# Performance work log

Hardware: AMD Instinct MI355X
Metric: run time of the kernel (lower is better)

The kernel has to match this reference:

```python
import jax, jax.numpy as jnp
import numpy as np

B = 4096
OBS, ACT, RDIM = 128, 32, 4
HID = 1024                      # embedding output / head hidden dim
DIMS = [OBS + ACT + RDIM, 128, 128, RDIM]   # target net: 164 -> 128 -> 128 -> 4
N_LAYERS = len(DIMS) - 1


def setup_inputs() -> dict:
    key = jax.random.key(0)
    ks = iter(jax.random.split(key, 64))

    def p(shape, scale=0.02):
        return jax.random.normal(next(ks), shape, jnp.float32) * scale

    inp = {
        "obs": jax.random.normal(next(ks), (B, OBS), jnp.float32),
        "action": jax.random.normal(next(ks), (B, ACT), jnp.float32),
        "prefs": jax.random.uniform(next(ks), (B, RDIM), jnp.float32),
        # embedding MLP (hypernet): (obs, prefs) -> z
        "We1": p((OBS + RDIM, HID)), "be1": jnp.zeros((HID,), jnp.float32),
        "We2": p((HID, HID)), "be2": jnp.zeros((HID,), jnp.float32),
    }
    # head nets: per target layer, linear heads emitting weight / bias / scale
    for i in range(N_LAYERS):
        din, dout = DIMS[i], DIMS[i + 1]
        inp[f"Ww{i}"] = p((HID, dout * din))
        inp[f"bw{i}"] = jnp.zeros((dout * din,), jnp.float32)
        inp[f"Wb{i}"] = p((HID, dout))
        inp[f"bb{i}"] = jnp.zeros((dout,), jnp.float32)
        inp[f"Ws{i}"] = p((HID, dout))
        inp[f"bs{i}"] = jnp.ones((dout,), jnp.float32)  # scale ~ 1 at init
    return inp


def reference(obs, action, prefs, We1, be1, We2, be2,
              Ww0, bw0, Wb0, bb0, Ws0, bs0,
              Ww1, bw1, Wb1, bb1, Ws1, bs1,
              Ww2, bw2, Wb2, bb2, Ws2, bs2):
    # hypernet embedding z  (hypernet_inputs = [obs, prefs])
    hin = jnp.concatenate([obs, prefs], axis=-1)          # [B, 132]
    z = jax.nn.relu(hin @ We1 + be1)
    z = jax.nn.relu(z @ We2 + be2)                        # [B, HID]

    heads = [(Ww0, bw0, Wb0, bb0, Ws0, bs0),
             (Ww1, bw1, Wb1, bb1, Ws1, bs1),
             (Ww2, bw2, Wb2, bb2, Ws2, bs2)]

    # target network input (target_net_inputs = [obs, action, prefs])
    x = jnp.concatenate([obs, action, prefs], axis=-1)    # [B, 164]

    for i, (Ww, bw, Wb, bb, Ws, bs) in enumerate(heads):
        din, dout = DIMS[i], DIMS[i + 1]
        w = (z @ Ww + bw).reshape(-1, dout, din)          # per-sample [B, dout, din]
        b = z @ Wb + bb                                   # [B, dout]
        s = z @ Ws + bs                                   # [B, dout]
        x = (jnp.einsum('bi,boi->bo', x, w) + b) * s      # batched matmul+bias+scale
        if i < N_LAYERS - 1:                              # activation_mask: all but last
            x = jax.nn.relu(x)
    return x                                              # [B, reward_dim]
```

## Files before the change

### kernel.cpp

```cpp
#include <hip/hip_runtime.h>
#include <hip/hip_bf16.h>
#include <stdint.h>

#define B4 4096
#define KZ 1088
#define KH 160

typedef short bf16x8 __attribute__((ext_vector_type(8)));
typedef float f32x4 __attribute__((ext_vector_type(4)));

__device__ __forceinline__ float b2f(uint16_t u){
  union {float f; uint32_t i;} v; v.i = ((uint32_t)u)<<16; return v.f;
}
__device__ __forceinline__ uint16_t f2b(float f){
  union {float fv; uint32_t i;} v; v.fv = f;
  uint32_t r = v.i + 0x7FFFu + ((v.i>>16)&1u);
  return (uint16_t)(r>>16);
}
__device__ __forceinline__ void gload16(const void* g, void* l){
  __builtin_amdgcn_global_load_lds(
      (__attribute__((address_space(1))) void*)(g),
      (__attribute__((address_space(3))) void*)(l), 16, 0, 0);
}

__global__ __launch_bounds__(256) void transpose_pack(
    const float* __restrict__ src, const float* __restrict__ bias,
    uint16_t* __restrict__ dst,
    int Ncols, int Kdst, int Ksrc, int src_ld, int din_dst, int din_src)
{
  __shared__ float tile[32][33];
  int ct = blockIdx.x, kt = blockIdx.y;
  int tid = threadIdx.x;
  int cl = tid & 31, kg = tid >> 5;
  #pragma unroll
  for (int r = 0; r < 4; ++r){
    int kl = kg*4 + r;
    int k  = kt*32 + kl;
    int c  = ct*32 + cl;
    float v = 0.f;
    if (c < Ncols){
      int o = c / din_dst, i = c - o*din_dst;
      if (i < din_src){
        int sc = o*din_src + i;
        if (k < Ksrc)       v = src[(size_t)k*src_ld + sc];
        else if (k == Ksrc) v = bias[sc];
      }
    }
    tile[kl][cl] = v;
  }
  __syncthreads();
  int c_loc = tid >> 3, kq = tid & 7;
  int c = ct*32 + c_loc;
  if (c < Ncols){
    ushort4 st;
    uint16_t* sp = (uint16_t*)&st;
    #pragma unroll
    for (int r = 0; r < 4; ++r) sp[r] = f2b(tile[kq*4 + r][c_loc]);
    *(ushort4*)&dst[(size_t)c*Kdst + kt*32 + kq*4] = st;
  }
}

__global__ __launch_bounds__(256) void pack_hin(
    const float* __restrict__ obs, const float* __restrict__ prefs,
    uint16_t* __restrict__ hinp)
{
  int idx = blockIdx.x*256 + threadIdx.x;
  int b = idx / KH, k = idx - b*KH;
  float v;
  if (k < 128)      v = obs[b*128 + k];
  else if (k < 132) v = prefs[b*4 + (k-128)];
  else              v = (k == 132) ? 1.f : 0.f;
  hinp[idx] = f2b(v);
}

__global__ __launch_bounds__(256) void pack_x0T(
    const float* __restrict__ obs, const float* __restrict__ act,
    const float* __restrict__ prefs, uint16_t* __restrict__ x0T)
{
  int idx = blockIdx.x*256 + threadIdx.x;
  int c = idx >> 12;
  int b = idx & (B4-1);
  float v = 0.f;
  if (c < 128)      v = obs[b*128 + c];
  else if (c < 160) v = act[b*32 + (c-128)];
  else if (c < 164) v = prefs[b*4 + (c-160)];
  x0T[idx] = f2b(v);
}

__global__ __launch_bounds__(256) void zinit(uint16_t* __restrict__ z1p,
                                             uint16_t* __restrict__ zp)
{
  int idx = blockIdx.x*256 + threadIdx.x;
  int t = idx & 127;
  int row = idx >> 7;
  uint16_t* p = (t < 64) ? z1p : zp;
  int col = 1024 + (t & 63);
  p[(size_t)row*KZ + col] = ((t & 63) == 0) ? (uint16_t)0x3F80 : (uint16_t)0;
}

template<int RELU, int OUTBF, int TRANS>
__global__ __launch_bounds__(256) void gemm128(
    const uint16_t* __restrict__ A, int lda,
    const uint16_t* __restrict__ BT, int ldb,
    void* __restrict__ Cv, int ldc, int K)
{
  __shared__ char smA[128*64];
  __shared__ char smB[128*64];
  int tid = threadIdx.x, w = tid >> 6, lane = tid & 63;
  int m0 = blockIdx.x*128, n0 = blockIdx.y*128;
  const uint16_t* Ab = A  + (size_t)m0*lda;
  const uint16_t* Bb = BT + (size_t)n0*ldb;
  f32x4 acc[2][8];
  #pragma unroll
  for (int mf = 0; mf < 2; ++mf)
    #pragma unroll
    for (int nf = 0; nf < 8; ++nf) acc[mf][nf] = (f32x4){0.f,0.f,0.f,0.f};
  int colg = lane & 15, hi = lane >> 4;

  for (int k0 = 0; k0 < K; k0 += 32){
    #pragma unroll
    for (int p = 0; p < 2; ++p){
      int rb = p*4 + w;
      int row = rb*16 + (lane >> 2);
      int chunk = (lane & 3) ^ ((row >> 1) & 3);
      gload16(Ab + (size_t)row*lda + k0 + chunk*8, &smA[rb*1024]);
      gload16(Bb + (size_t)row*ldb + k0 + chunk*8, &smB[rb*1024]);
    }
    __syncthreads();
    bf16x8 af[2];
    #pragma unroll
    for (int mf = 0; mf < 2; ++mf){
      int row = w*32 + mf*16 + colg;
      af[mf] = *(const bf16x8*)&smA[row*64 + ((hi ^ ((row>>1)&3)) << 4)];
    }
    #pragma unroll
    for (int nf = 0; nf < 8; ++nf){
      int row = nf*16 + colg;
      bf16x8 bfr = *(const bf16x8*)&smB[row*64 + ((hi ^ ((row>>1)&3)) << 4)];
      acc[0][nf] = __builtin_amdgcn_mfma_f32_16x16x32_bf16(af[0], bfr, acc[0][nf], 0,0,0);
      acc[1][nf] = __builtin_amdgcn_mfma_f32_16x16x32_bf16(af[1], bfr, acc[1][nf], 0,0,0);
    }
    __syncthreads();
  }
  #pragma unroll
  for (int mf = 0; mf < 2; ++mf){
    #pragma unroll
    for (int nf = 0; nf < 8; ++nf){
      int col = n0 + nf*16 + colg;
      #pragma unroll
      for (int r = 0; r < 4; ++r){
        int row = m0 + w*32 + mf*16 + hi*4 + r;
        float v = acc[mf][nf][r];
        if (RELU) v = v > 0.f ? v : 0.f;
        if (TRANS)      ((float*)Cv)[(size_t)col*ldc + row] = v;
        else if (OUTBF) ((uint16_t*)Cv)[(size_t)row*ldc + col] = f2b(v);
        else            ((float*)Cv)[(size_t)row*ldc + col] = v;
      }
    }
  }
}

template<int DINP>
__global__ __launch_bounds__(512, 2) void hyper2n(
    const uint16_t* __restrict__ zp,
    const uint16_t* __restrict__ WpT,
    const uint16_t* __restrict__ xT,
    const float*  __restrict__ bsbT,
    uint16_t* __restrict__ outT,
    int relu)
{
  constexpr int NF     = DINP/32;
  constexpr int BCALLS = DINP/64;
  constexpr int WAITN  = 2 + BCALLS;
  constexpr int HBUF   = 16384 + 2*DINP*64;
  constexpr int NH     = KZ/32;
  __shared__ char sm[3*HBUF];

  int tid = threadIdx.x, w = tid >> 6, lane = tid & 63;
  int wm = w >> 2, wn = w & 3;
  int f = blockIdx.x;
  int xcd = f & 7;
  int j = f >> 3;
  int pair = j >> 1;
  int mt = xcd*2 + (j & 1);
  int m0 = mt*256;
  const uint16_t* Ag = zp  + (size_t)m0*KZ;
  const uint16_t* Bg = WpT + (size_t)pair*(2*DINP)*KZ;
  int colg = lane & 15, hi = lane >> 4;

  f32x4 acc[8][NF];
  #pragma unroll
  for (int mf = 0; mf < 8; ++mf)
    #pragma unroll
    for (int nf = 0; nf < NF; ++nf) acc[mf][nf] = (f32x4){0.f,0.f,0.f,0.f};

  auto SA = [&](int h, int a){
    int row = a*128 + (tid >> 2);
    int ch  = (tid & 3) ^ ((row >> 1) & 3);
    gload16(Ag + (size_t)row*KZ + h*32 + ch*8,
            sm + (h%3)*HBUF + a*8192 + w*1024);
  };
  auto SB = [&](int h, int b){
    int row = b*128 + (tid >> 2);
    int ch  = (tid & 3) ^ ((row >> 1) & 3);
    gload16(Bg + (size_t)row*KZ + h*32 + ch*8,
            sm + (h%3)*HBUF + 16384 + b*8192 + w*1024);
  };

  SA(0,0); SA(0,1);
  #pragma unroll
  for (int b = 0; b < BCALLS; ++b) SB(0,b);
  SA(1,0); SA(1,1);
  #pragma unroll
  for (int b = 0; b < BCALLS; ++b) SB(1,b);

  for (int h = 0; h < NH; ++h){
    const char* base = sm + (h%3)*HBUF;
    if (h == NH-1) asm volatile("s_waitcnt vmcnt(0)" ::: "memory");
    else           asm volatile("s_waitcnt vmcnt(%0)" :: "i"(WAITN) : "memory");
    __builtin_amdgcn_s_barrier();
    if (h + 2 < NH){
      SA(h+2,0); SA(h+2,1);
      #pragma unroll
      for (int b = 0; b < BCALLS; ++b) SB(h+2,b);
    }
    bf16x8 Bf[NF];
    #pragma unroll
    for (int nf = 0; nf < NF; ++nf){
      int rc = wn*(DINP/2) + nf*16 + colg;
      Bf[nf] = *(const bf16x8*)(base + 16384 + rc*64 + ((hi ^ ((rc>>1)&3)) << 4));
    }
    #pragma unroll
    for (int m = 0; m < 8; ++m){
      int row = wm*128 + m*16 + colg;
      bf16x8 a = *(const bf16x8*)(base + row*64 + ((hi ^ ((row>>1)&3)) << 4));
      #pragma unroll
      for (int nf = 0; nf < NF; ++nf)
        acc[m][nf] = __builtin_amdgcn_mfma_f32_16x16x32_bf16(a, Bf[nf], acc[m][nf], 0,0,0);
    }
  }

  __syncthreads();
  float* red = (float*)sm;
  int parity = wn & 1, o_loc = wn >> 1;
  #pragma unroll
  for (int mf = 0; mf < 8; ++mf){
    float p0=0.f, p1=0.f, p2=0.f, p3=0.f;
    int b0 = m0 + wm*128 + mf*16 + hi*4;
    #pragma unroll
    for (int nf = 0; nf < NF; ++nf){
      int il = parity*(DINP/2) + nf*16 + colg;
      ushort4 xv = *(const ushort4*)(xT + (size_t)il*B4 + b0);
      f32x4 a = acc[mf][nf];
      p0 += a[0]*b2f(xv.x); p1 += a[1]*b2f(xv.y);
      p2 += a[2]*b2f(xv.z); p3 += a[3]*b2f(xv.w);
    }
    #pragma unroll
    for (int off = 1; off < 16; off <<= 1){
      p0 += __shfl_xor(p0, off); p1 += __shfl_xor(p1, off);
      p2 += __shfl_xor(p2, off); p3 += __shfl_xor(p3, off);
    }
    if (colg == 0){
      int rloc = wm*128 + mf*16 + hi*4;
      float* rp = red + parity*512 + o_loc*256 + rloc;
      rp[0] = p0; rp[1] = p1; rp[2] = p2; rp[3] = p3;
    }
  }
  __syncthreads();
  {
    int o_l = tid >> 8, row = tid & 255;
    int o = pair*2 + o_l;
    float v = red[o_l*256 + row] + red[512 + o_l*256 + row];
    float bv = bsbT[(size_t)o*B4 + m0 + row];
    float sv = bsbT[(size_t)(128+o)*B4 + m0 + row];
    float val = (v + bv) * sv;
    if (relu) val = val > 0.f ? val : 0.f;
    outT[(size_t)o*B4 + m0 + row] = f2b(val);
  }
}

__global__ __launch_bounds__(256) void finalize_k(
    const float* __restrict__ w2, const uint16_t* __restrict__ x2T,
    const float* __restrict__ bs2, float* __restrict__ out)
{
  int tid = threadIdx.x;
  int o = tid & 3;
  int b = blockIdx.x*64 + (tid >> 2);
  const float* wr = w2 + (size_t)b*512 + o*128;
  float dot = 0.f;
  #pragma unroll
  for (int i = 0; i < 128; i += 4){
    float4 wv = *(const float4*)(wr + i);
    dot += wv.x * b2f(x2T[(size_t)(i+0)*B4 + b]);
    dot += wv.y * b2f(x2T[(size_t)(i+1)*B4 + b]);
    dot += wv.z * b2f(x2T[(size_t)(i+2)*B4 + b]);
    dot += wv.w * b2f(x2T[(size_t)(i+3)*B4 + b]);
  }
  float bv = bs2[(size_t)b*128 + o];
  float sv = bs2[(size_t)b*128 + 4 + o];
  out[b*4 + o] = (dot + bv) * sv;
}

extern "C" void kernel_launch(void* const* d_in, const int* in_sizes, int n_in,
                              void* d_out, int out_size, void* d_ws, size_t ws_size,
                              hipStream_t stream)
{
  const float* obs   = (const float*)d_in[0];
  const float* act   = (const float*)d_in[1];
  const float* prefs = (const float*)d_in[2];
  const float* We1 = (const float*)d_in[3];
  const float* be1 = (const float*)d_in[4];
  const float* We2 = (const float*)d_in[5];
  const float* be2 = (const float*)d_in[6];
  const float* Ww0 = (const float*)d_in[7],  *bw0 = (const float*)d_in[8];
  const float* Wb0 = (const float*)d_in[9],  *bb0 = (const float*)d_in[10];
  const float* Ws0 = (const float*)d_in[11], *bs0i = (const float*)d_in[12];
  const float* Ww1 = (const float*)d_in[13], *bw1 = (const float*)d_in[14];
  const float* Wb1 = (const float*)d_in[15], *bb1 = (const float*)d_in[16];
  const float* Ws1 = (const float*)d_in[17], *bs1i = (const float*)d_in[18];
  const float* Ww2 = (const float*)d_in[19], *bw2 = (const float*)d_in[20];
  const float* Wb2 = (const float*)d_in[21], *bb2 = (const float*)d_in[22];
  const float* Ws2 = (const float*)d_in[23], *bs2i = (const float*)d_in[24];

  char* ws = (char*)d_ws;
  size_t off = 0;
  auto alloc = [&](size_t bytes)->char*{
    char* p = ws + off; off += (bytes + 255) & ~(size_t)255; return p;
  };
  uint16_t* WpT0  = (uint16_t*)alloc((size_t)24576*KZ*2);
  uint16_t* WpT1  = (uint16_t*)alloc((size_t)16384*KZ*2);
  uint16_t* WpT2  = (uint16_t*)alloc((size_t)512*KZ*2);
  uint16_t* We1T  = (uint16_t*)alloc((size_t)1024*KH*2);
  uint16_t* We2T  = (uint16_t*)alloc((size_t)1024*KZ*2);
  uint16_t* Wbs0T = (uint16_t*)alloc((size_t)256*KZ*2);
  uint16_t* Wbs1T = (uint16_t*)alloc((size_t)256*KZ*2);
  uint16_t* Wbs2T = (uint16_t*)alloc((size_t)128*KZ*2);
  uint16_t* hinp  = (uint16_t*)alloc((size_t)B4*KH*2);
  uint16_t* z1p   = (uint16_t*)alloc((size_t)B4*KZ*2);
  uint16_t* zp    = (uint16_t*)alloc((size_t)B4*KZ*2);
  float*    bsb0  = (float*)alloc((size_t)256*B4*4);
  float*    bsb1  = (float*)alloc((size_t)256*B4*4);
  float*    bsb2  = (float*)alloc((size_t)B4*128*4);
  uint16_t* x0T   = (uint16_t*)alloc((size_t)192*B4*2);
  uint16_t* x1T   = (uint16_t*)alloc((size_t)128*B4*2);
  uint16_t* x2T   = (uint16_t*)alloc((size_t)128*B4*2);
  float*    w2    = (float*)alloc((size_t)B4*512*4);
  (void)ws_size; (void)in_sizes; (void)n_in; (void)out_size;

  hipMemsetAsync(Wbs2T, 0, (size_t)128*KZ*2, stream);

  dim3 blk(256);
  auto tg = [](int nc, int kd){ return dim3((nc+31)/32, kd/32); };
  transpose_pack<<<tg(24576,KZ),blk,0,stream>>>(Ww0, bw0, WpT0, 24576, KZ, 1024, 20992, 192, 164);
  transpose_pack<<<tg(16384,KZ),blk,0,stream>>>(Ww1, bw1, WpT1, 16384, KZ, 1024, 16384, 128, 128);
  transpose_pack<<<tg(512,KZ),blk,0,stream>>>(Ww2, bw2, WpT2, 512, KZ, 1024, 512, 128, 128);
  transpose_pack<<<tg(1024,KH),blk,0,stream>>>(We1, be1, We1T, 1024, KH, 132, 1024, 1024, 1024);
  transpose_pack<<<tg(1024,KZ),blk,0,stream>>>(We2, be2, We2T, 1024, KZ, 1024, 1024, 1024, 1024);
  transpose_pack<<<tg(128,KZ),blk,0,stream>>>(Wb0, bb0, Wbs0T,          128, KZ, 1024, 128, 128, 128);
  transpose_pack<<<tg(128,KZ),blk,0,stream>>>(Ws0, bs0i, Wbs0T + 128*KZ,128, KZ, 1024, 128, 128, 128);
  transpose_pack<<<tg(128,KZ),blk,0,stream>>>(Wb1, bb1, Wbs1T,          128, KZ, 1024, 128, 128, 128);
  transpose_pack<<<tg(128,KZ),blk,0,stream>>>(Ws1, bs1i, Wbs1T + 128*KZ,128, KZ, 1024, 128, 128, 128);
  transpose_pack<<<tg(4,KZ),blk,0,stream>>>(Wb2, bb2, Wbs2T,        4, KZ, 1024, 4, 4, 4);
  transpose_pack<<<tg(4,KZ),blk,0,stream>>>(Ws2, bs2i, Wbs2T + 4*KZ,4, KZ, 1024, 4, 4, 4);

  pack_hin<<<dim3(B4*KH/256),blk,0,stream>>>(obs, prefs, hinp);
  pack_x0T<<<dim3(192*B4/256),blk,0,stream>>>(obs, act, prefs, x0T);
  zinit<<<dim3(B4*128/256),blk,0,stream>>>(z1p, zp);

  gemm128<1,1,0><<<dim3(32,8),blk,0,stream>>>(hinp, KH, We1T, KH, z1p, KZ, KH);
  gemm128<1,1,0><<<dim3(32,8),blk,0,stream>>>(z1p, KZ, We2T, KZ, zp, KZ, KZ);
  gemm128<0,0,1><<<dim3(32,4),blk,0,stream>>>(zp, KZ, Wbs0T, KZ, bsb0, B4, KZ);
  gemm128<0,0,0><<<dim3(32,1),blk,0,stream>>>(zp, KZ, Wbs2T, KZ, bsb2, 128, KZ);

  hyper2n<192><<<dim3(1024),dim3(512),0,stream>>>(zp, WpT0, x0T, bsb0, x1T, 1);
  hyper2n<128><<<dim3(1024),dim3(512),0,stream>>>(zp, WpT1, x1T, bsb1, x2T, 1);

  gemm128<0,0,0><<<dim3(32,4),blk,0,stream>>>(zp, KZ, WpT2, KZ, w2, 512, KZ);
  finalize_k<<<dim3(B4/64),blk,0,stream>>>(w2, x2T, bsb2, (float*)d_out);
}
```

Baseline: 603.2 us.

## Shrink padded K, merge packing kernels, and precompute hyper2n load addresses

Reduces the padded inner dimension KZ from 1088 to 1056, cutting the wasted K work and bytes in every z-based GEMM. It also merges the six small bias/scale transpose launches into one kernel, and the three input-packing launches into one. The hyper2n main loop now uses precomputed pointers and LDS offsets with a 3-way unrolled ring buffer, replacing the per-iteration address math. Risks: NH must be divisible by 3 for the unrolled loop, Wbs1T is no longer written, and correctness depends on the bias layout still matching hyper2n.

```diff
diff --git a/kernel.cpp b/kernel.cpp
--- a/kernel.cpp
+++ b/kernel.cpp
@@ -3,7 +3,7 @@
 #include <stdint.h>
 
 #define B4 4096
-#define KZ 1088
+#define KZ 1056
 #define KH 160
 
 typedef short bf16x8 __attribute__((ext_vector_type(8)));
@@ -60,42 +60,86 @@
   }
 }
 
-__global__ __launch_bounds__(256) void pack_hin(
-    const float* __restrict__ obs, const float* __restrict__ prefs,
-    uint16_t* __restrict__ hinp)
-{
-  int idx = blockIdx.x*256 + threadIdx.x;
-  int b = idx / KH, k = idx - b*KH;
-  float v;
-  if (k < 128)      v = obs[b*128 + k];
-  else if (k < 132) v = prefs[b*4 + (k-128)];
-  else              v = (k == 132) ? 1.f : 0.f;
-  hinp[idx] = f2b(v);
-}
-
-__global__ __launch_bounds__(256) void pack_x0T(
+__global__ __launch_bounds__(256) void transpose_pack_bs(
+    const float* __restrict__ Wb0, const float* __restrict__ bb0,
+    const float* __restrict__ Ws0, const float* __restrict__ bs0,
+    const float* __restrict__ Wb1, const float* __restrict__ bb1,
+    const float* __restrict__ Ws1, const float* __restrict__ bs1,
+    const float* __restrict__ Wb2, const float* __restrict__ bb2,
+    const float* __restrict__ Ws2, const float* __restrict__ bs2,
+    uint16_t* __restrict__ WbsT, uint16_t* __restrict__ Wbs2T)
+{
+  __shared__ float tile[32][33];
+  int ct = blockIdx.x, kt = blockIdx.y;
+  int tid = threadIdx.x;
+  int cl = tid & 31, kg = tid >> 5;
+  #pragma unroll
+  for (int r = 0; r < 4; ++r){
+    int kl = kg*4 + r;
+    int k  = kt*32 + kl;
+    int c  = ct*32 + cl;
+    float v = 0.f;
+    if (c < 512){
+      int sel = c >> 7, sc = c & 127;
+      const float* S  = (sel==0) ? Wb0 : (sel==1) ? Ws0 : (sel==2) ? Wb1 : Ws1;
+      const float* Bs = (sel==0) ? bb0 : (sel==1) ? bs0 : (sel==2) ? bb1 : bs1;
+      if (k < 1024)       v = S[(size_t)k*128 + sc];
+      else if (k == 1024) v = Bs[sc];
+    } else if (c < 520){
+      int cc = c - 512;
+      int sel = cc >> 2, sc = cc & 3;
+      const float* S  = sel ? Ws2 : Wb2;
+      const float* Bs = sel ? bs2 : bb2;
+      if (k < 1024)       v = S[(size_t)k*4 + sc];
+      else if (k == 1024) v = Bs[sc];
+    }
+    tile[kl][cl] = v;
+  }
+  __syncthreads();
+  int c_loc = tid >> 3, kq = tid & 7;
+  int c = ct*32 + c_loc;
+  if (c < 520){
+    ushort4 st;
+    uint16_t* sp = (uint16_t*)&st;
+    #pragma unroll
+    for (int r = 0; r < 4; ++r) sp[r] = f2b(tile[kq*4 + r][c_loc]);
+    uint16_t* dst = (c < 512) ? &WbsT[(size_t)c*KZ] : &Wbs2T[(size_t)(c-512)*KZ];
+    *(ushort4*)&dst[kt*32 + kq*4] = st;
+  }
+}
+
+__global__ __launch_bounds__(256) void pack_misc(
     const float* __restrict__ obs, const float* __restrict__ act,
-    const float* __restrict__ prefs, uint16_t* __restrict__ x0T)
-{
-  int idx = blockIdx.x*256 + threadIdx.x;
-  int c = idx >> 12;
-  int b = idx & (B4-1);
-  float v = 0.f;
-  if (c < 128)      v = obs[b*128 + c];
-  else if (c < 160) v = act[b*32 + (c-128)];
-  else if (c < 164) v = prefs[b*4 + (c-160)];
-  x0T[idx] = f2b(v);
-}
-
-__global__ __launch_bounds__(256) void zinit(uint16_t* __restrict__ z1p,
-                                             uint16_t* __restrict__ zp)
-{
-  int idx = blockIdx.x*256 + threadIdx.x;
-  int t = idx & 127;
-  int row = idx >> 7;
-  uint16_t* p = (t < 64) ? z1p : zp;
-  int col = 1024 + (t & 63);
-  p[(size_t)row*KZ + col] = ((t & 63) == 0) ? (uint16_t)0x3F80 : (uint16_t)0;
+    const float* __restrict__ prefs,
+    uint16_t* __restrict__ hinp, uint16_t* __restrict__ x0T,
+    uint16_t* __restrict__ z1p, uint16_t* __restrict__ zp)
+{
+  int bid = blockIdx.x;
+  if (bid < 2560){
+    int idx = bid*256 + threadIdx.x;
+    int b = idx / KH, k = idx - b*KH;
+    float v;
+    if (k < 128)      v = obs[b*128 + k];
+    else if (k < 132) v = prefs[b*4 + (k-128)];
+    else              v = (k == 132) ? 1.f : 0.f;
+    hinp[idx] = f2b(v);
+  } else if (bid < 5632){
+    int idx = (bid-2560)*256 + threadIdx.x;
+    int c = idx >> 12;
+    int b = idx & (B4-1);
+    float v = 0.f;
+    if (c < 128)      v = obs[b*128 + c];
+    else if (c < 160) v = act[b*32 + (c-128)];
+    else if (c < 164) v = prefs[b*4 + (c-160)];
+    x0T[idx] = f2b(v);
+  } else {
+    int idx = (bid-5632)*256 + threadIdx.x;
+    int t = idx & 63;
+    int row = idx >> 6;
+    uint16_t* p = (t < 32) ? z1p : zp;
+    int col = 1024 + (t & 31);
+    p[(size_t)row*KZ + col] = ((t & 31) == 0) ? (uint16_t)0x3F80 : (uint16_t)0;
+  }
 }
 
 template<int RELU, int OUTBF, int TRANS>
@@ -194,50 +238,69 @@
     #pragma unroll
     for (int nf = 0; nf < NF; ++nf) acc[mf][nf] = (f32x4){0.f,0.f,0.f,0.f};
 
-  auto SA = [&](int h, int a){
-    int row = a*128 + (tid >> 2);
-    int ch  = (tid & 3) ^ ((row >> 1) & 3);
-    gload16(Ag + (size_t)row*KZ + h*32 + ch*8,
-            sm + (h%3)*HBUF + a*8192 + w*1024);
-  };
-  auto SB = [&](int h, int b){
-    int row = b*128 + (tid >> 2);
-    int ch  = (tid & 3) ^ ((row >> 1) & 3);
-    gload16(Bg + (size_t)row*KZ + h*32 + ch*8,
-            sm + (h%3)*HBUF + 16384 + b*8192 + w*1024);
-  };
-
-  SA(0,0); SA(0,1);
-  #pragma unroll
-  for (int b = 0; b < BCALLS; ++b) SB(0,b);
-  SA(1,0); SA(1,1);
-  #pragma unroll
-  for (int b = 0; b < BCALLS; ++b) SB(1,b);
-
-  for (int h = 0; h < NH; ++h){
-    const char* base = sm + (h%3)*HBUF;
+  int rA0 = tid >> 2;
+  int rA1 = 128 + rA0;
+  const uint16_t* srcA0 = Ag + (size_t)rA0*KZ + (((tid&3) ^ ((rA0>>1)&3))*8);
+  const uint16_t* srcA1 = Ag + (size_t)rA1*KZ + (((tid&3) ^ ((rA1>>1)&3))*8);
+  const uint16_t* srcB[BCALLS];
+  #pragma unroll
+  for (int b = 0; b < BCALLS; ++b){
+    int rb = b*128 + (tid >> 2);
+    srcB[b] = Bg + (size_t)rb*KZ + (((tid&3) ^ ((rb>>1)&3))*8);
+  }
+  int dA0 = w*1024;
+  int dA1 = 8192 + w*1024;
+  int dB0 = 16384 + w*1024;
+
+  int offB[NF], offA[8];
+  #pragma unroll
+  for (int nf = 0; nf < NF; ++nf){
+    int rc = wn*(DINP/2) + nf*16 + colg;
+    offB[nf] = 16384 + rc*64 + ((hi ^ ((rc>>1)&3)) << 4);
+  }
+  #pragma unroll
+  for (int m = 0; m < 8; ++m){
+    int row = wm*128 + m*16 + colg;
+    offA[m] = row*64 + ((hi ^ ((row>>1)&3)) << 4);
+  }
+
+  gload16(srcA0,      sm + dA0);  gload16(srcA1,      sm + dA1);
+  #pragma unroll
+  for (int b = 0; b < BCALLS; ++b) gload16(srcB[b],      sm + dB0 + b*8192);
+  gload16(srcA0 + 32, sm + HBUF + dA0);  gload16(srcA1 + 32, sm + HBUF + dA1);
+  #pragma unroll
+  for (int b = 0; b < BCALLS; ++b) gload16(srcB[b] + 32, sm + HBUF + dB0 + b*8192);
+
+  auto ITER = [&](int h, char* base, char* pf){
     if (h == NH-1) asm volatile("s_waitcnt vmcnt(0)" ::: "memory");
     else           asm volatile("s_waitcnt vmcnt(%0)" :: "i"(WAITN) : "memory");
     __builtin_amdgcn_s_barrier();
     if (h + 2 < NH){
-      SA(h+2,0); SA(h+2,1);
+      gload16(srcA0 + 64, pf + dA0);
+      gload16(srcA1 + 64, pf + dA1);
       #pragma unroll
-      for (int b = 0; b < BCALLS; ++b) SB(h+2,b);
-    }
+      for (int b = 0; b < BCALLS; ++b) gload16(srcB[b] + 64, pf + dB0 + b*8192);
+    }
+    srcA0 += 32; srcA1 += 32;
+    #pragma unroll
+    for (int b = 0; b < BCALLS; ++b) srcB[b] += 32;
     bf16x8 Bf[NF];
     #pragma unroll
-    for (int nf = 0; nf < NF; ++nf){
-      int rc = wn*(DINP/2) + nf*16 + colg;
-      Bf[nf] = *(const bf16x8*)(base + 16384 + rc*64 + ((hi ^ ((rc>>1)&3)) << 4));
-    }
+    for (int nf = 0; nf < NF; ++nf)
+      Bf[nf] = *(const bf16x8*)(base + offB[nf]);
     #pragma unroll
     for (int m = 0; m < 8; ++m){
-      int row = wm*128 + m*16 + colg;
-      bf16x8 a = *(const bf16x8*)(base + row*64 + ((hi ^ ((row>>1)&3)) << 4));
+      bf16x8 a = *(const bf16x8*)(base + offA[m]);
       #pragma unroll
       for (int nf = 0; nf < NF; ++nf)
         acc[m][nf] = __builtin_amdgcn_mfma_f32_16x16x32_bf16(a, Bf[nf], acc[m][nf], 0,0,0);
     }
+  };
+
+  for (int hh = 0; hh < NH; hh += 3){
+    ITER(hh,     sm,            sm + 2*HBUF);
+    ITER(hh + 1, sm + HBUF,     sm);
+    ITER(hh + 2, sm + 2*HBUF,   sm + HBUF);
   }
 
   __syncthreads();
@@ -346,6 +409,7 @@
   uint16_t* x2T   = (uint16_t*)alloc((size_t)128*B4*2);
   float*    w2    = (float*)alloc((size_t)B4*512*4);
   (void)ws_size; (void)in_sizes; (void)n_in; (void)out_size;
+  (void)Wbs1T;
 
   hipMemsetAsync(Wbs2T, 0, (size_t)128*KZ*2, stream);
 
@@ -356,16 +420,11 @@
   transpose_pack<<<tg(512,KZ),blk,0,stream>>>(Ww2, bw2, WpT2, 512, KZ, 1024, 512, 128, 128);
   transpose_pack<<<tg(1024,KH),blk,0,stream>>>(We1, be1, We1T, 1024, KH, 132, 1024, 1024, 1024);
   transpose_pack<<<tg(1024,KZ),blk,0,stream>>>(We2, be2, We2T, 1024, KZ, 1024, 1024, 1024, 1024);
-  transpose_pack<<<tg(128,KZ),blk,0,stream>>>(Wb0, bb0, Wbs0T,          128, KZ, 1024, 128, 128, 128);
-  transpose_pack<<<tg(128,KZ),blk,0,stream>>>(Ws0, bs0i, Wbs0T + 128*KZ,128, KZ, 1024, 128, 128, 128);
-  transpose_pack<<<tg(128,KZ),blk,0,stream>>>(Wb1, bb1, Wbs1T,          128, KZ, 1024, 128, 128, 128);
-  transpose_pack<<<tg(128,KZ),blk,0,stream>>>(Ws1, bs1i, Wbs1T + 128*KZ,128, KZ, 1024, 128, 128, 128);
-  transpose_pack<<<tg(4,KZ),blk,0,stream>>>(Wb2, bb2, Wbs2T,        4, KZ, 1024, 4, 4, 4);
-  transpose_pack<<<tg(4,KZ),blk,0,stream>>>(Ws2, bs2i, Wbs2T + 4*KZ,4, KZ, 1024, 4, 4, 4);
-
-  pack_hin<<<dim3(B4*KH/256),blk,0,stream>>>(obs, prefs, hinp);
-  pack_x0T<<<dim3(192*B4/256),blk,0,stream>>>(obs, act, prefs, x0T);
-  zinit<<<dim3(B4*128/256),blk,0,stream>>>(z1p, zp);
+  transpose_pack_bs<<<dim3(17,KZ/32),blk,0,stream>>>(
+      Wb0, bb0, Ws0, bs0i, Wb1, bb1, Ws1, bs1i, Wb2, bb2, Ws2, bs2i,
+      Wbs0T, Wbs2T);
+
+  pack_misc<<<dim3(6656),blk,0,stream>>>(obs, act, prefs, hinp, x0T, z1p, zp);
 
   gemm128<1,1,0><<<dim3(32,8),blk,0,stream>>>(hinp, KH, We1T, KH, z1p, KZ, KH);
   gemm128<1,1,0><<<dim3(32,8),blk,0,stream>>>(z1p, KZ, We2T, KZ, zp, KZ, KZ);
```

Result: slower. 816.2 us (+35.3%).
